# Performance work log

Measured on AMD Instinct MI355X. Metric: run time of the kernel, lower is better.

The kernel has to match this reference:

```python
import jax, jax.numpy as jnp
import numpy as np

NUM_HEADS = 32
NUM_KV_HEADS = 8
HEAD_DIM = 128
HIDDEN = 4096
THETA = 10000.0


def apply_rotary_emb(x, theta=THETA):
    # x: (B, S, H, D). Torch code converts to complex with real = first half
    # of last dim, imag = second half (rotate-half convention).
    B, S, H, D = x.shape
    half = D // 2
    freqs = 1.0 / theta ** (jnp.arange(0, D, 2, dtype=jnp.float32) / D)  # (half,)
    t = jnp.arange(S, dtype=jnp.float32)
    ang = jnp.outer(t, freqs)  # (S, half)
    cos = jnp.cos(ang)[None, :, None, :]  # (1,S,1,half)
    sin = jnp.sin(ang)[None, :, None, :]
    x1, x2 = x[..., :half], x[..., half:]
    out = jnp.concatenate([x1 * cos - x2 * sin, x1 * sin + x2 * cos], axis=-1)
    return out.astype(x.dtype)


def setup_inputs() -> dict:
    key = jax.random.key(0)
    k1, k2, k3 = jax.random.split(key, 3)
    B, S = 1, 2048
    qkv_out = (NUM_HEADS + 2 * NUM_KV_HEADS) * HEAD_DIM  # 6144
    hidden_states = jax.random.normal(k1, (B, S, HIDDEN), dtype=jnp.float32)
    w_qkv = jax.random.normal(k2, (qkv_out, HIDDEN), dtype=jnp.float32) * 0.02
    w_o = jax.random.normal(k3, (HIDDEN, NUM_HEADS * HEAD_DIM), dtype=jnp.float32) * 0.02
    return {"hidden_states": hidden_states, "w_qkv": w_qkv, "w_o": w_o}


def reference(hidden_states, w_qkv, w_o):
    B, S, _ = hidden_states.shape
    q_size = NUM_HEADS * HEAD_DIM
    kv_size = NUM_KV_HEADS * HEAD_DIM
    n_rep = NUM_HEADS // NUM_KV_HEADS

    qkv = hidden_states @ w_qkv.T  # (B,S,6144)
    xq = qkv[..., :q_size].reshape(B, S, NUM_HEADS, HEAD_DIM)
    xk = qkv[..., q_size:q_size + kv_size].reshape(B, S, NUM_KV_HEADS, HEAD_DIM)
    xv = qkv[..., q_size + kv_size:].reshape(B, S, NUM_KV_HEADS, HEAD_DIM)

    xq = apply_rotary_emb(xq)
    xk = apply_rotary_emb(xk)

    # repeat_interleave KV heads to match query heads
    xk = jnp.repeat(xk, n_rep, axis=2)
    xv = jnp.repeat(xv, n_rep, axis=2)

    q = xq.transpose(0, 2, 1, 3)  # (B,H,S,D)
    k = xk.transpose(0, 2, 1, 3)
    v = xv.transpose(0, 2, 1, 3)

    scale = 1.0 / np.sqrt(HEAD_DIM).astype(np.float32)
    scores = jnp.einsum('bhqd,bhkd->bhqk', q, k) * scale
    causal = jnp.tril(jnp.ones((S, S), dtype=bool))
    scores = jnp.where(causal[None, None], scores, jnp.float32(-jnp.inf))
    attn = jax.nn.softmax(scores, axis=-1)  # dropout=0 (eval)
    out = jnp.einsum('bhqk,bhkd->bhqd', attn, v)
    out = out.transpose(0, 2, 1, 3).reshape(B, S, NUM_HEADS * HEAD_DIM)
    return out @ w_o.T
```

## Files before the change

kernel.cpp:

```cpp
#include <hip/hip_runtime.h>
#include <cstdint>

#define S_LEN 2048
#define HID   4096
#define NHQ   32
#define NKV   8
#define HD    128
#define QKV_N 6144

typedef float  f32x4 __attribute__((ext_vector_type(4)));
typedef short  s16x8 __attribute__((ext_vector_type(8)));
typedef unsigned short ushort_t;

typedef __attribute__((address_space(3))) void       lds_void;
typedef const __attribute__((address_space(1))) void gbl_void;

__device__ __forceinline__ void gload_lds16(const void* g, void* l) {
  __builtin_amdgcn_global_load_lds((gbl_void*)g, (lds_void*)l, 16, 0, 0);
}

__device__ __forceinline__ short f2bf_bits(float f) {
  union { __bf16 b; short s; } u;
  u.b = (__bf16)f;
  return u.s;
}
__device__ __forceinline__ float bf2f(unsigned short u) {
  union { unsigned int i; float f; } x;
  x.i = ((unsigned int)u) << 16;
  return x.f;
}

__device__ __forceinline__ void cvt8(const float* src, ushort_t* dst, int j) {
  const f32x4* s = (const f32x4*)src;
  f32x4 a = s[j * 2], b = s[j * 2 + 1];
  s16x8 r;
  r[0] = f2bf_bits(a[0]); r[1] = f2bf_bits(a[1]); r[2] = f2bf_bits(a[2]); r[3] = f2bf_bits(a[3]);
  r[4] = f2bf_bits(b[0]); r[5] = f2bf_bits(b[1]); r[6] = f2bf_bits(b[2]); r[7] = f2bf_bits(b[3]);
  *((s16x8*)dst + j) = r;
}

__global__ __launch_bounds__(256)
void cvt_hw(const float* __restrict__ h, const float* __restrict__ wq,
            ushort_t* __restrict__ hb, ushort_t* __restrict__ wqb) {
  int i = blockIdx.x * 256 + threadIdx.x;
  if (i < 1048576) cvt8(h, hb, i);
  else             cvt8(wq, wqb, i - 1048576);
}

__device__ __forceinline__ s16x8 frag_b16(const ushort_t* tile, int row, int quad) {
  return *(const s16x8*)(tile + row * 32 + quad * 8);
}

template <bool OUTF32>
__global__ __launch_bounds__(256)
void gemm_bt_bf16(const ushort_t* __restrict__ Ag, const ushort_t* __restrict__ Bg,
                  void* __restrict__ Cp, int M, int N, int K) {
  __shared__ __align__(16) ushort_t As[2][128 * 32];
  __shared__ __align__(16) ushort_t Bs[2][128 * 32];
  const int t = threadIdx.x;
  const int w = t >> 6, l = t & 63;
  const int n16 = l & 15, quad = l >> 4;
  const int m0 = blockIdx.x * 128, n0 = blockIdx.y * 128;
  const int wm = (w >> 1) * 64, wn = (w & 1) * 64;

  const int sIdx0 = (w * 2 + 0) * 64 + l;
  const int sIdx1 = (w * 2 + 1) * 64 + l;
  const int aRow0 = sIdx0 >> 2, aCs0 = (sIdx0 & 3) * 8;
  const int aRow1 = sIdx1 >> 2, aCs1 = (sIdx1 & 3) * 8;
  const ushort_t* Arow0 = Ag + (size_t)(m0 + aRow0) * K + aCs0;
  const ushort_t* Arow1 = Ag + (size_t)(m0 + aRow1) * K + aCs1;
  const ushort_t* Brow0 = Bg + (size_t)(n0 + aRow0) * K + aCs0;
  const ushort_t* Brow1 = Bg + (size_t)(n0 + aRow1) * K + aCs1;

  f32x4 acc[4][4] = {};

  auto stage = [&](int k0, int buf) {
    gload_lds16(Arow0 + k0, (char*)&As[buf][0] + (w * 2 + 0) * 1024);
    gload_lds16(Arow1 + k0, (char*)&As[buf][0] + (w * 2 + 1) * 1024);
    gload_lds16(Brow0 + k0, (char*)&Bs[buf][0] + (w * 2 + 0) * 1024);
    gload_lds16(Brow1 + k0, (char*)&Bs[buf][0] + (w * 2 + 1) * 1024);
  };
  auto compute = [&](int buf) {
    s16x8 afr[4], bfr[4];
#pragma unroll
    for (int i = 0; i < 4; i++) afr[i] = frag_b16(&As[buf][0], wm + i * 16 + n16, quad);
#pragma unroll
    for (int j = 0; j < 4; j++) bfr[j] = frag_b16(&Bs[buf][0], wn + j * 16 + n16, quad);
#pragma unroll
    for (int i = 0; i < 4; i++)
#pragma unroll
      for (int j = 0; j < 4; j++)
        acc[i][j] = __builtin_amdgcn_mfma_f32_16x16x32_bf16(afr[i], bfr[j], acc[i][j], 0, 0, 0);
  };

  const int nIter = K >> 5;
  stage(0, 0);
  for (int it = 0; it < nIter; it += 2) {
    __syncthreads();
    if (it + 1 < nIter) stage((it + 1) << 5, 1);
    compute(0);
    __syncthreads();
    if (it + 2 < nIter) stage((it + 2) << 5, 0);
    compute(1);
  }

#pragma unroll
  for (int i = 0; i < 4; i++)
#pragma unroll
    for (int j = 0; j < 4; j++)
#pragma unroll
      for (int r = 0; r < 4; r++) {
        int row = m0 + wm + i * 16 + quad * 4 + r;
        int col = n0 + wn + j * 16 + n16;
        float v = acc[i][j][r];
        if constexpr (OUTF32) ((float*)Cp)[(size_t)row * N + col] = v;
        else ((ushort_t*)Cp)[(size_t)row * N + col] = (ushort_t)f2bf_bits(v);
      }
}

__global__ __launch_bounds__(256)
void rope_vt_cvtwo(const ushort_t* __restrict__ qkv, ushort_t* __restrict__ Q,
                   ushort_t* __restrict__ Kc, ushort_t* __restrict__ Vt,
                   const float* __restrict__ wo, ushort_t* __restrict__ wob) {
  __shared__ __align__(16) ushort_t tile[64][72];
  const int b = blockIdx.x;
  const int t = threadIdx.x;
  if (b < 2048) {
    const int s = b;
    const float LN1E4_64 = 0.14391156831212787f;
    for (int item = t; item < (NHQ + NKV) * 64; item += 256) {
      int head = item >> 6, i = item & 63;
      float f = expf(-(float)i * LN1E4_64);
      float ang = (float)s * f;
      float sn, cs;
      sincosf(ang, &sn, &cs);
      if (head < NHQ) {
        const ushort_t* src = qkv + (size_t)s * QKV_N + head * HD;
        float x1 = bf2f(src[i]), x2 = bf2f(src[64 + i]);
        const float sc = 0.08838834764831845f;
        ushort_t* dst = Q + ((size_t)head * S_LEN + s) * HD;
        dst[i]      = (ushort_t)f2bf_bits((x1 * cs - x2 * sn) * sc);
        dst[64 + i] = (ushort_t)f2bf_bits((x1 * sn + x2 * cs) * sc);
      } else {
        int kv = head - NHQ;
        const ushort_t* src = qkv + (size_t)s * QKV_N + 4096 + kv * HD;
        float x1 = bf2f(src[i]), x2 = bf2f(src[64 + i]);
        ushort_t* dst = Kc + ((size_t)kv * S_LEN + s) * HD;
        dst[i]      = (ushort_t)f2bf_bits(x1 * cs - x2 * sn);
        dst[64 + i] = (ushort_t)f2bf_bits(x1 * sn + x2 * cs);
      }
    }
  } else if (b < 2560) {
    const int bb = b - 2048;
    const int s0 = (bb & 31) * 64;
    const int by = bb >> 5;
    const int kv = by >> 1;
    const int d0 = (by & 1) * 64;
    {
      int r = t >> 2, c = (t & 3) * 16;
      const ushort_t* src = qkv + (size_t)(s0 + r) * QKV_N + 5120 + kv * HD + d0 + c;
      *(s16x8*)&tile[r][c]     = *(const s16x8*)src;
      *(s16x8*)&tile[r][c + 8] = *(const s16x8*)(src + 8);
    }
    __syncthreads();
    {
      int d = t >> 2, sseg = (t & 3) * 16;
      ushort_t* dst = Vt + ((size_t)kv * HD + d0 + d) * S_LEN + s0 + sseg;
      s16x8 o1, o2;
#pragma unroll
      for (int i = 0; i < 8; i++) { o1[i] = tile[sseg + i][d]; o2[i] = tile[sseg + 8 + i][d]; }
      *(s16x8*)dst = o1;
      *(s16x8*)(dst + 8) = o2;
    }
  } else {
    int j = (b - 2560) * 256 + t;
    cvt8(wo, wob, j);
  }
}

__global__ __launch_bounds__(256)
void attn_kernel(const ushort_t* __restrict__ Q, const ushort_t* __restrict__ Kc,
                 const ushort_t* __restrict__ Vt, ushort_t* __restrict__ Out) {
  __shared__ __align__(16) ushort_t Ks[2][64 * 128];
  __shared__ __align__(16) ushort_t Vs[2][128 * 64];
  __shared__ __align__(16) ushort_t Pl[4][16 * 72];
  const int bx = blockIdx.x;
  const int h = blockIdx.y;
  const int t = threadIdx.x, w = t >> 6, l = t & 63;
  const int n16 = l & 15, quad = l >> 4;
  const int kv = h >> 2;
  const ushort_t* Qh = Q  + (size_t)h  * S_LEN * HD;
  const ushort_t* Kh = Kc + (size_t)kv * S_LEN * HD;
  const ushort_t* Vh = Vt + (size_t)kv * HD * S_LEN;

  const int qtA = bx, qtB = 31 - bx;
  const int q0A = qtA * 64 + w * 16, q0B = qtB * 64 + w * 16;
  const int tripsA = qtA + 1;
  const int TOTAL = 33;

  s16x8 qfA[4], qfB[4];
#pragma unroll
  for (int ks = 0; ks < 4; ks++) {
    qfA[ks] = *(const s16x8*)(Qh + (size_t)(q0A + n16) * HD + ks * 32 + quad * 8);
    qfB[ks] = *(const s16x8*)(Qh + (size_t)(q0B + n16) * HD + ks * 32 + quad * 8);
  }

  s16x8 ones;
  {
    short v = (n16 == 0) ? (short)0x3F80 : (short)0;
#pragma unroll
    for (int j = 0; j < 8; j++) ones[j] = v;
  }

  f32x4 o[9] = {};
  float mrun[4] = {-1e30f, -1e30f, -1e30f, -1e30f};

  ushort_t* P = Pl[w];

  auto stage = [&](int k0, int buf) {
#pragma unroll
    for (int c = 0; c < 4; c++) {
      int idx = (c * 4 + w) * 64 + l;
      int row = idx >> 4, sc = idx & 15;
      int dseg = sc ^ (row & 15);
      gload_lds16(Kh + (size_t)(k0 + row) * HD + dseg * 8,
                  (char*)&Ks[buf][0] + (c * 4 + w) * 1024);
    }
#pragma unroll
    for (int c = 0; c < 4; c++) {
      int idx = (c * 4 + w) * 64 + l;
      int row = idx >> 3, sc = idx & 7;
      int ks2 = sc ^ (row & 7);
      gload_lds16(Vh + (size_t)row * S_LEN + k0 + ks2 * 8,
                  (char*)&Vs[buf][0] + (c * 4 + w) * 1024);
    }
  };

  stage(0, 0);

  for (int i = 0; i < TOTAL; i++) {
    const bool isA = (i < tripsA);
    const int kt = isA ? i : i - tripsA;
    const int q0 = isA ? q0A : q0B;
    const int k0 = kt * 64;
    const int buf = i & 1;

    __syncthreads();

    if (i + 1 < TOTAL) {
      const bool nA = (i + 1 < tripsA);
      const int nkt = nA ? (i + 1) : (i + 1 - tripsA);
      stage(nkt * 64, buf ^ 1);
    }

    const ushort_t* KsB = &Ks[buf][0];
    const ushort_t* VsB = &Vs[buf][0];

    f32x4 sacc[4] = {};
#pragma unroll
    for (int ks = 0; ks < 4; ks++) {
      s16x8 qf = isA ? qfA[ks] : qfB[ks];
#pragma unroll
      for (int nt = 0; nt < 4; nt++) {
        int row = nt * 16 + n16;
        s16x8 kf = *(const s16x8*)(KsB + row * 128 + ((ks * 4 + quad) ^ (row & 15)) * 8);
        sacc[nt] = __builtin_amdgcn_mfma_f32_16x16x32_bf16(qf, kf, sacc[nt], 0, 0, 0);
      }
    }

    if (k0 + 63 > q0) {
#pragma unroll
      for (int nt = 0; nt < 4; nt++)
#pragma unroll
        for (int r = 0; r < 4; r++) {
          int qrow = q0 + quad * 4 + r;
          int key  = k0 + nt * 16 + n16;
          if (key > qrow) sacc[nt][r] = -1e30f;
        }
    }

#pragma unroll
    for (int r = 0; r < 4; r++) {
      float tmx = fmaxf(fmaxf(sacc[0][r], sacc[1][r]), fmaxf(sacc[2][r], sacc[3][r]));
#pragma unroll
      for (int d = 1; d < 16; d <<= 1) tmx = fmaxf(tmx, __shfl_xor(tmx, d));
      float nm = fmaxf(mrun[r], tmx);
      float alpha = __expf(mrun[r] - nm);
      mrun[r] = nm;
#pragma unroll
      for (int nt = 0; nt < 4; nt++) sacc[nt][r] = __expf(sacc[nt][r] - nm);
#pragma unroll
      for (int nt2 = 0; nt2 < 9; nt2++) o[nt2][r] *= alpha;
    }

#pragma unroll
    for (int nt = 0; nt < 4; nt++)
#pragma unroll
      for (int r = 0; r < 4; r++)
        P[(quad * 4 + r) * 72 + nt * 16 + n16] = (ushort_t)f2bf_bits(sacc[nt][r]);
    asm volatile("s_waitcnt lgkmcnt(0)" ::: "memory");
    s16x8 pa[2];
#pragma unroll
    for (int kseg = 0; kseg < 2; kseg++)
      pa[kseg] = *(const s16x8*)(P + n16 * 72 + kseg * 32 + quad * 8);

#pragma unroll
    for (int kseg = 0; kseg < 2; kseg++) {
#pragma unroll
      for (int ntd = 0; ntd < 8; ntd++) {
        int row = ntd * 16 + n16;
        s16x8 vf = *(const s16x8*)(VsB + row * 64 + ((kseg * 4 + quad) ^ (row & 7)) * 8);
        o[ntd] = __builtin_amdgcn_mfma_f32_16x16x32_bf16(pa[kseg], vf, o[ntd], 0, 0, 0);
      }
      o[8] = __builtin_amdgcn_mfma_f32_16x16x32_bf16(pa[kseg], ones, o[8], 0, 0, 0);
    }

    if (i == tripsA - 1) {
#pragma unroll
      for (int r = 0; r < 4; r++) {
        float lsum = __shfl(o[8][r], l & 48);
        float inv = 1.0f / lsum;
        int qrow = q0A + quad * 4 + r;
#pragma unroll
        for (int ntd = 0; ntd < 8; ntd++)
          Out[(size_t)qrow * HID + h * HD + ntd * 16 + n16] = (ushort_t)f2bf_bits(o[ntd][r] * inv);
      }
#pragma unroll
      for (int nt2 = 0; nt2 < 9; nt2++) o[nt2] = (f32x4){0.f, 0.f, 0.f, 0.f};
#pragma unroll
      for (int r = 0; r < 4; r++) mrun[r] = -1e30f;
    }
  }

#pragma unroll
  for (int r = 0; r < 4; r++) {
    float lsum = __shfl(o[8][r], l & 48);
    float inv = 1.0f / lsum;
    int qrow = q0B + quad * 4 + r;
#pragma unroll
    for (int ntd = 0; ntd < 8; ntd++)
      Out[(size_t)qrow * HID + h * HD + ntd * 16 + n16] = (ushort_t)f2bf_bits(o[ntd][r] * inv);
  }
}

extern "C" void kernel_launch(void* const* d_in, const int* in_sizes, int n_in,
                              void* d_out, int out_size, void* d_ws, size_t ws_size,
                              hipStream_t stream) {
  const float* hidden = (const float*)d_in[0];
  const float* w_qkv  = (const float*)d_in[1];
  const float* w_o    = (const float*)d_in[2];
  float* out = (float*)d_out;
  char* ws = (char*)d_ws;

  ushort_t* hidden_bf = (ushort_t*)ws;
  ushort_t* Qb        = (ushort_t*)ws;
  ushort_t* wqkv_bf   = (ushort_t*)(ws + 16777216);
  ushort_t* wo_bf     = (ushort_t*)(ws + 16777216);
  ushort_t* qkv       = (ushort_t*)(ws + 67108864);
  ushort_t* attn_out  = (ushort_t*)(ws + 67108864);
  ushort_t* Kb        = (ushort_t*)(ws + 92274688);
  ushort_t* Vtb       = (ushort_t*)(ws + 96468992);

  cvt_hw<<<dim3(16384), 256, 0, stream>>>(hidden, w_qkv, hidden_bf, wqkv_bf);
  gemm_bt_bf16<false><<<dim3(16, 48), 256, 0, stream>>>(hidden_bf, wqkv_bf, (void*)qkv, 2048, 6144, 4096);
  rope_vt_cvtwo<<<dim3(10752), 256, 0, stream>>>(qkv, Qb, Kb, Vtb, w_o, wo_bf);
  attn_kernel<<<dim3(16, 32), 256, 0, stream>>>(Qb, Kb, Vtb, attn_out);
  gemm_bt_bf16<true><<<dim3(16, 32), 256, 0, stream>>>(attn_out, wo_bf, (void*)out, 2048, 4096, 4096);
}
```

Baseline: 509.3 us.

## Replace GEMM with 4-stage ring-buffered, swizzled, larger-tile bf16 MFMA kernel

Replaces the double-buffered 128x128 GEMM with a 512-thread kernel that uses 256-wide N tiles (BM 256 or 128) and a 4-slot LDS ring that keeps three k-stages in flight. Each step is gated by explicit vmcnt waits and a single barrier, where the old kernel used two syncthreads per pair. LDS rows are XOR-swizzled to avoid bank conflicts, and MFMA blocks are issued at raised priority. The aim is to hide global-load latency and raise per-block reuse for both projection GEMMs. In exchange it uses more LDS and registers per block, which may limit occupancy, and it launches fewer blocks (192 and 256).

```diff
diff --git a/kernel.cpp b/kernel.cpp
--- a/kernel.cpp
+++ b/kernel.cpp
@@ -47,72 +47,100 @@
   else             cvt8(wq, wqb, i - 1048576);
 }
 
-__device__ __forceinline__ s16x8 frag_b16(const ushort_t* tile, int row, int quad) {
-  return *(const s16x8*)(tile + row * 32 + quad * 8);
-}
-
-template <bool OUTF32>
-__global__ __launch_bounds__(256)
-void gemm_bt_bf16(const ushort_t* __restrict__ Ag, const ushort_t* __restrict__ Bg,
-                  void* __restrict__ Cp, int M, int N, int K) {
-  __shared__ __align__(16) ushort_t As[2][128 * 32];
-  __shared__ __align__(16) ushort_t Bs[2][128 * 32];
+template <int N> __device__ __forceinline__ void wait_vm() {
+  if constexpr (N == 8)      asm volatile("s_waitcnt vmcnt(8)" ::: "memory");
+  else if constexpr (N == 6) asm volatile("s_waitcnt vmcnt(6)" ::: "memory");
+  else if constexpr (N == 4) asm volatile("s_waitcnt vmcnt(4)" ::: "memory");
+  else if constexpr (N == 3) asm volatile("s_waitcnt vmcnt(3)" ::: "memory");
+  else                       asm volatile("s_waitcnt vmcnt(0)" ::: "memory");
+}
+
+template <int BM, bool OUTF32>
+__global__ __launch_bounds__(512, 2)
+void gemm_ring(const ushort_t* __restrict__ Ag, const ushort_t* __restrict__ Bg,
+               void* __restrict__ Cp, int M, int N, int K) {
+  constexpr int ALD = BM / 128;
+  constexpr int PHL = ALD + 2;
+  constexpr int MF  = BM / 32;
+  __shared__ __align__(16) ushort_t As[4][BM * 32];
+  __shared__ __align__(16) ushort_t Bs[4][256 * 32];
+
   const int t = threadIdx.x;
   const int w = t >> 6, l = t & 63;
   const int n16 = l & 15, quad = l >> 4;
-  const int m0 = blockIdx.x * 128, n0 = blockIdx.y * 128;
-  const int wm = (w >> 1) * 64, wn = (w & 1) * 64;
-
-  const int sIdx0 = (w * 2 + 0) * 64 + l;
-  const int sIdx1 = (w * 2 + 1) * 64 + l;
-  const int aRow0 = sIdx0 >> 2, aCs0 = (sIdx0 & 3) * 8;
-  const int aRow1 = sIdx1 >> 2, aCs1 = (sIdx1 & 3) * 8;
-  const ushort_t* Arow0 = Ag + (size_t)(m0 + aRow0) * K + aCs0;
-  const ushort_t* Arow1 = Ag + (size_t)(m0 + aRow1) * K + aCs1;
-  const ushort_t* Brow0 = Bg + (size_t)(n0 + aRow0) * K + aCs0;
-  const ushort_t* Brow1 = Bg + (size_t)(n0 + aRow1) * K + aCs1;
-
-  f32x4 acc[4][4] = {};
-
-  auto stage = [&](int k0, int buf) {
-    gload_lds16(Arow0 + k0, (char*)&As[buf][0] + (w * 2 + 0) * 1024);
-    gload_lds16(Arow1 + k0, (char*)&As[buf][0] + (w * 2 + 1) * 1024);
-    gload_lds16(Brow0 + k0, (char*)&Bs[buf][0] + (w * 2 + 0) * 1024);
-    gload_lds16(Brow1 + k0, (char*)&Bs[buf][0] + (w * 2 + 1) * 1024);
+  const int wm = w >> 2, wn = w & 3;
+  const int sw = quad ^ (n16 & 3);
+  const int m0 = blockIdx.x * BM, n0 = blockIdx.y * 256;
+
+  size_t aoff[ALD]; int aldo[ALD];
+#pragma unroll
+  for (int n2 = 0; n2 < ALD; n2++) {
+    int li = n2 * 512 + t, row = li >> 2, q = (li & 3) ^ (row & 3);
+    aoff[n2] = (size_t)(m0 + row) * K + q * 8;
+    aldo[n2] = li * 16;
+  }
+  size_t boff[2]; int bldo[2];
+#pragma unroll
+  for (int n2 = 0; n2 < 2; n2++) {
+    int li = n2 * 512 + t, row = li >> 2, q = (li & 3) ^ (row & 3);
+    boff[n2] = (size_t)(n0 + row) * K + q * 8;
+    bldo[n2] = li * 16;
+  }
+
+  f32x4 acc[MF][4] = {};
+
+  auto stage = [&](int slot, int k0) {
+#pragma unroll
+    for (int n2 = 0; n2 < ALD; n2++)
+      gload_lds16(Ag + aoff[n2] + k0, (char*)&As[slot][0] + aldo[n2]);
+#pragma unroll
+    for (int n2 = 0; n2 < 2; n2++)
+      gload_lds16(Bg + boff[n2] + k0, (char*)&Bs[slot][0] + bldo[n2]);
   };
-  auto compute = [&](int buf) {
-    s16x8 afr[4], bfr[4];
-#pragma unroll
-    for (int i = 0; i < 4; i++) afr[i] = frag_b16(&As[buf][0], wm + i * 16 + n16, quad);
-#pragma unroll
-    for (int j = 0; j < 4; j++) bfr[j] = frag_b16(&Bs[buf][0], wn + j * 16 + n16, quad);
-#pragma unroll
-    for (int i = 0; i < 4; i++)
-#pragma unroll
-      for (int j = 0; j < 4; j++)
-        acc[i][j] = __builtin_amdgcn_mfma_f32_16x16x32_bf16(afr[i], bfr[j], acc[i][j], 0, 0, 0);
+
+  auto compute = [&](int slot) {
+    const char* Ab = (const char*)&As[slot][0];
+    const char* Bb = (const char*)&Bs[slot][0];
+    s16x8 af[MF], bfr[4];
+#pragma unroll
+    for (int mf = 0; mf < MF; mf++)
+      af[mf] = *(const s16x8*)(Ab + (wm * (BM / 2) + mf * 16 + n16) * 64 + sw * 16);
+#pragma unroll
+    for (int nf = 0; nf < 4; nf++)
+      bfr[nf] = *(const s16x8*)(Bb + (wn * 64 + nf * 16 + n16) * 64 + sw * 16);
+    __builtin_amdgcn_s_setprio(1);
+#pragma unroll
+    for (int mf = 0; mf < MF; mf++)
+#pragma unroll
+      for (int nf = 0; nf < 4; nf++)
+        acc[mf][nf] = __builtin_amdgcn_mfma_f32_16x16x32_bf16(af[mf], bfr[nf], acc[mf][nf], 0, 0, 0);
+    __builtin_amdgcn_s_setprio(0);
   };
 
-  const int nIter = K >> 5;
-  stage(0, 0);
-  for (int it = 0; it < nIter; it += 2) {
-    __syncthreads();
-    if (it + 1 < nIter) stage((it + 1) << 5, 1);
-    compute(0);
-    __syncthreads();
-    if (it + 2 < nIter) stage((it + 2) << 5, 0);
-    compute(1);
-  }
-
-#pragma unroll
-  for (int i = 0; i < 4; i++)
-#pragma unroll
-    for (int j = 0; j < 4; j++)
+  const int NS = K >> 5;
+  stage(0, 0); stage(1, 32); stage(2, 64);
+  wait_vm<2 * PHL>();
+  __builtin_amdgcn_s_barrier();
+  asm volatile("" ::: "memory");
+
+  for (int s = 0; s < NS; ++s) {
+    if (s + 3 < NS) stage((s + 3) & 3, (s + 3) << 5);
+    compute(s & 3);
+    if (s <= NS - 4)      wait_vm<2 * PHL>();
+    else if (s == NS - 3) wait_vm<PHL>();
+    else if (s == NS - 2) wait_vm<0>();
+    if (s != NS - 1) { __builtin_amdgcn_s_barrier(); asm volatile("" ::: "memory"); }
+  }
+
+#pragma unroll
+  for (int mf = 0; mf < MF; mf++)
+#pragma unroll
+    for (int nf = 0; nf < 4; nf++)
 #pragma unroll
       for (int r = 0; r < 4; r++) {
-        int row = m0 + wm + i * 16 + quad * 4 + r;
-        int col = n0 + wn + j * 16 + n16;
-        float v = acc[i][j][r];
+        int row = m0 + wm * (BM / 2) + mf * 16 + quad * 4 + r;
+        int col = n0 + wn * 64 + nf * 16 + n16;
+        float v = acc[mf][nf][r];
         if constexpr (OUTF32) ((float*)Cp)[(size_t)row * N + col] = v;
         else ((ushort_t*)Cp)[(size_t)row * N + col] = (ushort_t)f2bf_bits(v);
       }
@@ -362,8 +390,8 @@
   ushort_t* Vtb       = (ushort_t*)(ws + 96468992);
 
   cvt_hw<<<dim3(16384), 256, 0, stream>>>(hidden, w_qkv, hidden_bf, wqkv_bf);
-  gemm_bt_bf16<false><<<dim3(16, 48), 256, 0, stream>>>(hidden_bf, wqkv_bf, (void*)qkv, 2048, 6144, 4096);
+  gemm_ring<256, false><<<dim3(8, 24), 512, 0, stream>>>(hidden_bf, wqkv_bf, (void*)qkv, 2048, 6144, 4096);
   rope_vt_cvtwo<<<dim3(10752), 256, 0, stream>>>(qkv, Qb, Kb, Vtb, w_o, wo_bf);
   attn_kernel<<<dim3(16, 32), 256, 0, stream>>>(Qb, Kb, Vtb, attn_out);
-  gemm_bt_bf16<true><<<dim3(16, 32), 256, 0, stream>>>(attn_out, wo_bf, (void*)out, 2048, 4096, 4096);
-}
+  gemm_ring<128, true><<<dim3(16, 16), 512, 0, stream>>>(attn_out, wo_bf, (void*)out, 2048, 4096, 4096);
+}
```

Result: slower. 572.3 us (+12.4%).

## Replace 128x128 GEMM with 256x256 8-wave pipelined swizzled kernel

Applied to the files above, without the earlier changes.

Replaces the simple double-buffered 128x128 bf16 GEMM with a 256x256 tile kernel using 512 threads (8 waves). It splits each K=64 tile into half-tiles loaded across eight phases with explicit vmcnt waits, XOR-swizzles LDS to avoid bank conflicts, and raises MFMA priority during compute. The aim is more data reuse per tile and better overlap of global->LDS loads with MFMA work. The cost is fewer blocks (192 and 128), which leaves the 256 CUs underfilled and adds a tail effect, plus higher register and LDS pressure.

```diff
diff --git a/kernel.cpp b/kernel.cpp
--- a/kernel.cpp
+++ b/kernel.cpp
@@ -47,72 +47,126 @@
   else             cvt8(wq, wqb, i - 1048576);
 }
 
-__device__ __forceinline__ s16x8 frag_b16(const ushort_t* tile, int row, int quad) {
-  return *(const s16x8*)(tile + row * 32 + quad * 8);
+template <int N> __device__ __forceinline__ void wait_vm() {
+  if constexpr (N == 6)      asm volatile("s_waitcnt vmcnt(6)" ::: "memory");
+  else if constexpr (N == 4) asm volatile("s_waitcnt vmcnt(4)" ::: "memory");
+  else                       asm volatile("s_waitcnt vmcnt(0)" ::: "memory");
 }
 
 template <bool OUTF32>
-__global__ __launch_bounds__(256)
-void gemm_bt_bf16(const ushort_t* __restrict__ Ag, const ushort_t* __restrict__ Bg,
-                  void* __restrict__ Cp, int M, int N, int K) {
-  __shared__ __align__(16) ushort_t As[2][128 * 32];
-  __shared__ __align__(16) ushort_t Bs[2][128 * 32];
+__global__ __launch_bounds__(512, 2)
+void gemm8p(const ushort_t* __restrict__ Ag, const ushort_t* __restrict__ Bg,
+            void* __restrict__ Cp, int M, int N, int K) {
+  __shared__ __align__(16) ushort_t As[2][2][256 * 32];
+  __shared__ __align__(16) ushort_t Bs[2][2][256 * 32];
+
   const int t = threadIdx.x;
   const int w = t >> 6, l = t & 63;
   const int n16 = l & 15, quad = l >> 4;
-  const int m0 = blockIdx.x * 128, n0 = blockIdx.y * 128;
-  const int wm = (w >> 1) * 64, wn = (w & 1) * 64;
-
-  const int sIdx0 = (w * 2 + 0) * 64 + l;
-  const int sIdx1 = (w * 2 + 1) * 64 + l;
-  const int aRow0 = sIdx0 >> 2, aCs0 = (sIdx0 & 3) * 8;
-  const int aRow1 = sIdx1 >> 2, aCs1 = (sIdx1 & 3) * 8;
-  const ushort_t* Arow0 = Ag + (size_t)(m0 + aRow0) * K + aCs0;
-  const ushort_t* Arow1 = Ag + (size_t)(m0 + aRow1) * K + aCs1;
-  const ushort_t* Brow0 = Bg + (size_t)(n0 + aRow0) * K + aCs0;
-  const ushort_t* Brow1 = Bg + (size_t)(n0 + aRow1) * K + aCs1;
-
-  f32x4 acc[4][4] = {};
-
-  auto stage = [&](int k0, int buf) {
-    gload_lds16(Arow0 + k0, (char*)&As[buf][0] + (w * 2 + 0) * 1024);
-    gload_lds16(Arow1 + k0, (char*)&As[buf][0] + (w * 2 + 1) * 1024);
-    gload_lds16(Brow0 + k0, (char*)&Bs[buf][0] + (w * 2 + 0) * 1024);
-    gload_lds16(Brow1 + k0, (char*)&Bs[buf][0] + (w * 2 + 1) * 1024);
+  const int wm = w >> 2, wn = w & 3;
+  const int sw16 = (quad ^ (n16 & 3)) * 16;
+  const int m0 = blockIdx.x * 256, n0 = blockIdx.y * 256;
+
+  const int srow = t >> 2;
+  const int schunk = (t & 3) ^ (srow & 3);
+  const ushort_t* Abase = Ag + (size_t)(m0 + srow) * K + schunk * 8;
+  const ushort_t* Bbase = Bg + (size_t)(n0 + srow) * K + schunk * 8;
+  char* AsB = (char*)&As[0][0][0];
+  char* BsB = (char*)&Bs[0][0][0];
+  const size_t hstep = (size_t)128 * K;
+
+  auto stageA = [&](int b, int h, int tile) {
+    const ushort_t* g = Abase + (size_t)h * hstep + tile * 64;
+    gload_lds16(g,      AsB + b * 32768 + h * 8192 + t * 16);
+    gload_lds16(g + 32, AsB + b * 32768 + 16384 + h * 8192 + t * 16);
   };
-  auto compute = [&](int buf) {
-    s16x8 afr[4], bfr[4];
-#pragma unroll
-    for (int i = 0; i < 4; i++) afr[i] = frag_b16(&As[buf][0], wm + i * 16 + n16, quad);
-#pragma unroll
-    for (int j = 0; j < 4; j++) bfr[j] = frag_b16(&Bs[buf][0], wn + j * 16 + n16, quad);
-#pragma unroll
-    for (int i = 0; i < 4; i++)
-#pragma unroll
-      for (int j = 0; j < 4; j++)
-        acc[i][j] = __builtin_amdgcn_mfma_f32_16x16x32_bf16(afr[i], bfr[j], acc[i][j], 0, 0, 0);
+  auto stageB = [&](int b, int h, int tile) {
+    const ushort_t* g = Bbase + (size_t)h * hstep + tile * 64;
+    gload_lds16(g,      BsB + b * 32768 + h * 8192 + t * 16);
+    gload_lds16(g + 32, BsB + b * 32768 + 16384 + h * 8192 + t * 16);
   };
 
-  const int nIter = K >> 5;
-  stage(0, 0);
-  for (int it = 0; it < nIter; it += 2) {
-    __syncthreads();
-    if (it + 1 < nIter) stage((it + 1) << 5, 1);
-    compute(0);
-    __syncthreads();
-    if (it + 2 < nIter) stage((it + 2) << 5, 0);
-    compute(1);
-  }
-
-#pragma unroll
-  for (int i = 0; i < 4; i++)
-#pragma unroll
-    for (int j = 0; j < 4; j++)
+  const int aRowBase = wm * 64 + n16;
+  const int bRowBase = wn * 32 + n16;
+  const char* AsR = (const char*)AsB;
+  const char* BsR = (const char*)BsB;
+
+  f32x4 acc[8][4] = {};
+  s16x8 af[4][2];
+
+#define PHASE(b, qm, qn, STAGE, WZ) do {                                            \
+    if ((qn) == 0) {                                                                \
+      _Pragma("unroll")                                                             \
+      for (int mf = 0; mf < 4; mf++)                                                \
+        _Pragma("unroll")                                                           \
+        for (int ks = 0; ks < 2; ks++)                                              \
+          af[mf][ks] = *(const s16x8*)(AsR + (b) * 32768 + ks * 16384 +             \
+                        ((qm) * 128 + mf * 16 + aRowBase) * 64 + sw16);             \
+    }                                                                               \
+    s16x8 bf[2][2];                                                                 \
+    _Pragma("unroll")                                                               \
+    for (int nf = 0; nf < 2; nf++)                                                  \
+      _Pragma("unroll")                                                             \
+      for (int ks = 0; ks < 2; ks++)                                                \
+        bf[nf][ks] = *(const s16x8*)(BsR + (b) * 32768 + ks * 16384 +               \
+                      ((qn) * 128 + nf * 16 + bRowBase) * 64 + sw16);               \
+    __builtin_amdgcn_s_setprio(1);                                                  \
+    _Pragma("unroll")                                                               \
+    for (int ks = 0; ks < 2; ks++)                                                  \
+      _Pragma("unroll")                                                             \
+      for (int mf = 0; mf < 4; mf++)                                                \
+        _Pragma("unroll")                                                           \
+        for (int nf = 0; nf < 2; nf++)                                              \
+          acc[(qm) * 4 + mf][(qn) * 2 + nf] = __builtin_amdgcn_mfma_f32_16x16x32_bf16( \
+              af[mf][ks], bf[nf][ks], acc[(qm) * 4 + mf][(qn) * 2 + nf], 0, 0, 0);  \
+    __builtin_amdgcn_s_setprio(0);                                                  \
+    STAGE;                                                                          \
+    if (WZ) wait_vm<0>(); else wait_vm<6>();                                        \
+    asm volatile("" ::: "memory");                                                  \
+    __builtin_amdgcn_s_barrier();                                                   \
+    asm volatile("" ::: "memory");                                                  \
+  } while (0)
+
+  const int NT = K >> 6;
+  const int NI = NT >> 1;
+
+  stageA(0, 0, 0); stageA(0, 1, 0); stageB(0, 0, 0); stageB(0, 1, 0);
+  stageA(1, 0, 1); stageB(1, 0, 1);
+  wait_vm<4>();
+  asm volatile("" ::: "memory");
+  __builtin_amdgcn_s_barrier();
+  asm volatile("" ::: "memory");
+
+  for (int i = 0; i < NI - 1; i++) {
+    const int tp1 = 2 * i + 1, tp2 = 2 * i + 2, tp3 = 2 * i + 3;
+    PHASE(0, 0, 0, stageA(1, 1, tp1), 0);
+    PHASE(0, 0, 1, stageB(1, 1, tp1), 0);
+    PHASE(0, 1, 0, stageA(0, 0, tp2), 0);
+    PHASE(0, 1, 1, stageB(0, 0, tp2), 0);
+    PHASE(1, 0, 0, stageA(0, 1, tp2), 0);
+    PHASE(1, 0, 1, stageB(0, 1, tp2), 0);
+    PHASE(1, 1, 0, stageA(1, 0, tp3), 0);
+    PHASE(1, 1, 1, stageB(1, 0, tp3), 0);
+  }
+  PHASE(0, 0, 0, stageA(1, 1, NT - 1), 0);
+  PHASE(0, 0, 1, stageB(1, 1, NT - 1), 0);
+  PHASE(0, 1, 0, ((void)0), 0);
+  PHASE(0, 1, 1, ((void)0), 1);
+  PHASE(1, 0, 0, ((void)0), 1);
+  PHASE(1, 0, 1, ((void)0), 1);
+  PHASE(1, 1, 0, ((void)0), 1);
+  PHASE(1, 1, 1, ((void)0), 1);
+#undef PHASE
+
+#pragma unroll
+  for (int a = 0; a < 8; a++)
+#pragma unroll
+    for (int bq = 0; bq < 4; bq++)
 #pragma unroll
       for (int r = 0; r < 4; r++) {
-        int row = m0 + wm + i * 16 + quad * 4 + r;
-        int col = n0 + wn + j * 16 + n16;
-        float v = acc[i][j][r];
+        int row = m0 + (a >> 2) * 128 + wm * 64 + (a & 3) * 16 + quad * 4 + r;
+        int col = n0 + (bq >> 1) * 128 + wn * 32 + (bq & 1) * 16 + n16;
+        float v = acc[a][bq][r];
         if constexpr (OUTF32) ((float*)Cp)[(size_t)row * N + col] = v;
         else ((ushort_t*)Cp)[(size_t)row * N + col] = (ushort_t)f2bf_bits(v);
       }
@@ -362,8 +416,8 @@
   ushort_t* Vtb       = (ushort_t*)(ws + 96468992);
 
   cvt_hw<<<dim3(16384), 256, 0, stream>>>(hidden, w_qkv, hidden_bf, wqkv_bf);
-  gemm_bt_bf16<false><<<dim3(16, 48), 256, 0, stream>>>(hidden_bf, wqkv_bf, (void*)qkv, 2048, 6144, 4096);
+  gemm8p<false><<<dim3(8, 24), 512, 0, stream>>>(hidden_bf, wqkv_bf, (void*)qkv, 2048, 6144, 4096);
   rope_vt_cvtwo<<<dim3(10752), 256, 0, stream>>>(qkv, Qb, Kb, Vtb, w_o, wo_bf);
   attn_kernel<<<dim3(16, 32), 256, 0, stream>>>(Qb, Kb, Vtb, attn_out);
-  gemm_bt_bf16<true><<<dim3(16, 32), 256, 0, stream>>>(attn_out, wo_bf, (void*)out, 2048, 4096, 4096);
-}
+  gemm8p<true><<<dim3(8, 16), 512, 0, stream>>>(attn_out, wo_bf, (void*)out, 2048, 4096, 4096);
+}
```

Result: slower. 560.2 us (+10.0%).
